# Kernel tuning notes

Measured on AMD Instinct MI355X. Metric: run time of the kernel, lower is better.

The kernel has to match this reference:

```python
import jax, jax.numpy as jnp
import numpy as np

B = 8192
H = 1024            # hidden_size
A = 512             # alphabet_size
S = 2               # sequence_length
D_IN = A * S        # 1024, gate input dim
D1, D2 = H // 2, H // 3   # decoder dims: 512, 341
TEMP = 1.0


def _linear_params(key, out_d, in_d):
    kw, kb = jax.random.split(key)
    lim = 1.0 / np.sqrt(in_d)
    W = jax.random.uniform(kw, (out_d, in_d), minval=-lim, maxval=lim, dtype=jnp.float32)
    b = jax.random.uniform(kb, (out_d,), minval=-lim, maxval=lim, dtype=jnp.float32)
    return W, b


def setup_inputs() -> dict:
    key = jax.random.key(0)
    ks = jax.random.split(key, 16)
    inp = {
        'x': jax.random.normal(ks[0], (B, D_IN), dtype=jnp.float32),
        'h': jax.random.normal(ks[1], (B, H), dtype=jnp.float32),
        'c': jax.random.normal(ks[2], (B, H), dtype=jnp.float32),
    }
    names = [('W_fi', 'b_fi', H, D_IN), ('W_fh', 'b_fh', H, H),
             ('W_ii', 'b_ii', H, D_IN), ('W_ih', 'b_ih', H, H),
             ('W_si', 'b_si', H, D_IN), ('W_sh', 'b_sh', H, H),
             ('W_oi', 'b_oi', H, D_IN), ('W_oh', 'b_oh', H, H),
             ('W_d1', 'b_d1', D1, H), ('W_d2', 'b_d2', D2, D1),
             ('W_d3', 'b_d3', A, D2)]
    for k, (wn, bn, od, idm) in zip(ks[3:3 + len(names)], names):
        W, b = _linear_params(k, od, idm)
        inp[wn] = W
        inp[bn] = b
    return inp


def reference(x, h, c,
              W_fi, b_fi, W_fh, b_fh,
              W_ii, b_ii, W_ih, b_ih,
              W_si, b_si, W_sh, b_sh,
              W_oi, b_oi, W_oh, b_oh,
              W_d1, b_d1, W_d2, b_d2, W_d3, b_d3):
    def lin(v, W, b):
        return v @ W.T + b

    f = jax.nn.sigmoid(lin(x, W_fi, b_fi) + lin(h, W_fh, b_fh))
    i = jax.nn.sigmoid(lin(x, W_ii, b_ii) + lin(h, W_ih, b_ih))
    s = jnp.tanh(lin(x, W_si, b_si) + lin(h, W_sh, b_sh))
    o = jax.nn.sigmoid(lin(x, W_oi, b_oi) + lin(h, W_oh, b_oh))
    c_new = c * f + i * s
    h_new = o * jnp.tanh(c_new)
    d = jnp.tanh(lin(h_new, W_d1, b_d1))
    d = jnp.tanh(lin(d, W_d2, b_d2))
    d = jax.nn.softmax(lin(d, W_d3, b_d3) / TEMP, axis=-1)
    return h_new, d
```

## Files before the change

### kernel.cpp

```cpp
#include <hip/hip_runtime.h>
#include <cstdint>
#include <cstddef>


typedef _Float16 half_t;
typedef _Float16 half8 __attribute__((ext_vector_type(8)));
typedef _Float16 half4v __attribute__((ext_vector_type(4)));
typedef float float4v __attribute__((ext_vector_type(4)));

#define GLD_LDS16(gptr, lptr)                                                  \
  __builtin_amdgcn_global_load_lds(                                            \
      (const __attribute__((address_space(1))) void*)(gptr),                   \
      (__attribute__((address_space(3))) void*)(lptr), 16, 0, 0)

__device__ __forceinline__ float fsig(float x) {
  return 1.0f / (1.0f + __expf(-x));
}
__device__ __forceinline__ float ftanh_(float x) {
  const float e = __expf(2.0f * x);
  return 1.0f - 2.0f / (e + 1.0f);
}

template <int TM, int ACT_TANH, int HALF_OUT>
__global__ __launch_bounds__(256) void gemm_f16(const half_t* __restrict__ A,
                                                const half_t* __restrict__ Bw,
                                                const float* __restrict__ bias,
                                                void* __restrict__ Cp,
                                                int N, int K) {
  constexpr int ASZ = TM * 64;
  constexpr int NPASS = (ASZ + 8192) / 4096;
  constexpr int JW = (TM == 128) ? 4 : 2;
  __shared__ alignas(16) half_t As[TM * 32];
  __shared__ alignas(16) half_t Bs[128 * 32];
  const int tid = threadIdx.x;
  const int lane = tid & 63;
  const int wave = tid >> 6;
  const size_t tile_m = (size_t)blockIdx.y * TM;
  const size_t tile_n = (size_t)blockIdx.x * 128;
  const int wm = (TM == 128) ? (wave >> 1) * 64 : 0;
  const int wn = (TM == 128) ? (wave & 1) * 64 : wave * 32;

  const half_t* gp[NPASS];
  half_t* lbase[NPASS];
  int lofs[NPASS];
#pragma unroll
  for (int s = 0; s < NPASS; ++s) {
    const int p = s * 4096 + tid * 16;
    if (p < ASZ) {
      const int r = p >> 6, cc = (p & 63) >> 1;
      gp[s] = A + (tile_m + r) * (size_t)K + cc;
      lbase[s] = As; lofs[s] = p;
    } else {
      const int q = p - ASZ;
      const int r = q >> 6, cc = (q & 63) >> 1;
      gp[s] = Bw + (tile_n + r) * (size_t)K + cc;
      lbase[s] = Bs; lofs[s] = q;
    }
  }

  float4v acc[4][JW] = {};
  for (int k0 = 0; k0 < K; k0 += 32) {
    __syncthreads();
#pragma unroll
    for (int s = 0; s < NPASS; ++s) GLD_LDS16(gp[s] + k0, (char*)lbase[s] + lofs[s]);
    __syncthreads();
    const int kh = (lane >> 4) * 8;
    half8 af[4], bf[JW];
#pragma unroll
    for (int i = 0; i < 4; ++i)
      af[i] = *(const half8*)(As + (wm + i * 16 + (lane & 15)) * 32 + kh);
#pragma unroll
    for (int j = 0; j < JW; ++j)
      bf[j] = *(const half8*)(Bs + (wn + j * 16 + (lane & 15)) * 32 + kh);
#pragma unroll
    for (int i = 0; i < 4; ++i)
#pragma unroll
      for (int j = 0; j < JW; ++j)
        acc[i][j] =
            __builtin_amdgcn_mfma_f32_16x16x32_f16(af[i], bf[j], acc[i][j], 0, 0, 0);
  }

  const size_t mb = tile_m + wm + ((lane >> 4) << 2);
  const size_t nb = tile_n + wn + (lane & 15);
#pragma unroll
  for (int j = 0; j < JW; ++j) {
    const size_t n = nb + j * 16;
    const float bv = bias[n];
#pragma unroll
    for (int i = 0; i < 4; ++i) {
#pragma unroll
      for (int r = 0; r < 4; ++r) {
        float v = acc[i][j][r] + bv;
        if (ACT_TANH) v = ftanh_(v);
        const size_t off = (mb + i * 16 + r) * (size_t)N + n;
        if (HALF_OUT)
          ((half_t*)Cp)[off] = (half_t)v;
        else
          ((float*)Cp)[off] = v;
      }
    }
  }
}

__global__ __launch_bounds__(256) void gemm_gates(const half_t* __restrict__ A,
                                                  const half_t* __restrict__ Bw,
                                                  const float* __restrict__ bias,
                                                  const float* __restrict__ cin,
                                                  float* __restrict__ hout,
                                                  half_t* __restrict__ h2) {
  constexpr int K = 2048;
  __shared__ alignas(16) half_t As[128 * 32];
  __shared__ alignas(16) half_t Bs[128 * 32];
  const int tid = threadIdx.x;
  const int lane = tid & 63;
  const int wave = tid >> 6;
  const size_t tile_m = (size_t)blockIdx.y * 128;
  const size_t tile_n = (size_t)blockIdx.x * 128;
  const int wm = (wave >> 1) * 64;
  const int wn = (wave & 1) * 64;

  const int p0 = tid * 16;
  const int p1 = 4096 + tid * 16;
  const int r0 = p0 >> 6, c0 = (p0 & 63) >> 1;
  const int r1 = p1 >> 6, c1 = (p1 & 63) >> 1;
  const half_t* Ag0 = A + (tile_m + r0) * (size_t)K + c0;
  const half_t* Ag1 = A + (tile_m + r1) * (size_t)K + c1;
  const half_t* Bg0 = Bw + (tile_n + r0) * (size_t)K + c0;
  const half_t* Bg1 = Bw + (tile_n + r1) * (size_t)K + c1;

  float4v acc[4][4] = {};
  for (int k0 = 0; k0 < K; k0 += 32) {
    __syncthreads();
    GLD_LDS16(Ag0 + k0, (char*)As + p0);
    GLD_LDS16(Ag1 + k0, (char*)As + p1);
    GLD_LDS16(Bg0 + k0, (char*)Bs + p0);
    GLD_LDS16(Bg1 + k0, (char*)Bs + p1);
    __syncthreads();
    const int kh = (lane >> 4) * 8;
    half8 af[4], bf[4];
#pragma unroll
    for (int i = 0; i < 4; ++i)
      af[i] = *(const half8*)(As + (wm + i * 16 + (lane & 15)) * 32 + kh);
#pragma unroll
    for (int j = 0; j < 4; ++j)
      bf[j] = *(const half8*)(Bs + (wn + j * 16 + (lane & 15)) * 32 + kh);
#pragma unroll
    for (int i = 0; i < 4; ++i)
#pragma unroll
      for (int j = 0; j < 4; ++j)
        acc[i][j] =
            __builtin_amdgcn_mfma_f32_16x16x32_f16(af[i], bf[j], acc[i][j], 0, 0, 0);
  }

  const int l = lane & 15;
  const int quad = lane >> 4;
  const int nwave = (int)tile_n + wn;
  const size_t u = (size_t)((nwave >> 6) << 4) + l;
  float bg[4];
#pragma unroll
  for (int g = 0; g < 4; ++g) bg[g] = bias[nwave + g * 16 + l];
#pragma unroll
  for (int i = 0; i < 4; ++i) {
#pragma unroll
    for (int r = 0; r < 4; ++r) {
      const size_t row = tile_m + wm + quad * 4 + i * 16 + r;
      const size_t off = row * 1024 + u;
      const float F = fsig(acc[i][0][r] + bg[0]);
      const float I = fsig(acc[i][1][r] + bg[1]);
      const float S = ftanh_(acc[i][2][r] + bg[2]);
      const float O = fsig(acc[i][3][r] + bg[3]);
      const float cn = cin[off] * F + I * S;
      const float hn = O * ftanh_(cn);
      hout[off] = hn;
      h2[off] = (half_t)hn;
    }
  }
}

__global__ void prep_pack(const float* __restrict__ x, const float* __restrict__ h,
                          const float* __restrict__ Wfi, const float* __restrict__ Wfh,
                          const float* __restrict__ Wii, const float* __restrict__ Wih,
                          const float* __restrict__ Wsi, const float* __restrict__ Wsh,
                          const float* __restrict__ Woi, const float* __restrict__ Woh,
                          half_t* __restrict__ xh, half_t* __restrict__ wall) {
  const int bid = blockIdx.x;
  const float* src;
  half_t* dst;
  size_t idx;
  if (bid < 16384) {
    idx = ((size_t)bid * 256 + threadIdx.x) * 4;
    const size_t b = idx >> 11;
    const int col = (int)(idx & 2047);
    src = (col < 1024) ? (x + b * 1024 + col) : (h + b * 1024 + (col - 1024));
    dst = xh + idx;
  } else {
    idx = ((size_t)(bid - 16384) * 256 + threadIdx.x) * 4;
    const int n = (int)(idx >> 11);
    const int col = (int)(idx & 2047);
    const int g = (n >> 4) & 3;
    const size_t u = (size_t)(((n >> 6) << 4) | (n & 15));
    const float* Wi = (g == 0) ? Wfi : (g == 1) ? Wii : (g == 2) ? Wsi : Woi;
    const float* Wh = (g == 0) ? Wfh : (g == 1) ? Wih : (g == 2) ? Wsh : Woh;
    src = (col < 1024) ? (Wi + u * 1024 + col) : (Wh + u * 1024 + (col - 1024));
    dst = wall + idx;
  }
  const float4v v = *(const float4v*)src;
  half4v o;
  o.x = (half_t)v.x; o.y = (half_t)v.y; o.z = (half_t)v.z; o.w = (half_t)v.w;
  *(half4v*)dst = o;
}

__global__ void prep_small(const float* __restrict__ Wd1, const float* __restrict__ Wd2,
                           const float* __restrict__ Wd3, const float* __restrict__ bd2,
                           const float* __restrict__ bfi, const float* __restrict__ bfh,
                           const float* __restrict__ bii, const float* __restrict__ bih,
                           const float* __restrict__ bsi, const float* __restrict__ bsh,
                           const float* __restrict__ boi, const float* __restrict__ boh,
                           half_t* __restrict__ WD1, half_t* __restrict__ WD2h,
                           half_t* __restrict__ WD3h, float* __restrict__ BALL,
                           float* __restrict__ BD2) {
  const int bid = blockIdx.x;
  const int tid = threadIdx.x;
  if (bid < 512) {
    const size_t i4 = ((size_t)bid * 256 + tid) * 4;
    const float4v v = *(const float4v*)(Wd1 + i4);
    half4v o;
    o.x = (half_t)v.x; o.y = (half_t)v.y; o.z = (half_t)v.z; o.w = (half_t)v.w;
    *(half4v*)(WD1 + i4) = o;
  } else if (bid < 704) {
    const size_t i4 = ((size_t)(bid - 512) * 256 + tid) * 4;
    const int r = (int)(i4 >> 9);
    const int cc = (int)(i4 & 511);
    half4v o;
    if (r < 341) {
      const float4v v = *(const float4v*)(Wd2 + (size_t)r * 512 + cc);
      o.x = (half_t)v.x; o.y = (half_t)v.y; o.z = (half_t)v.z; o.w = (half_t)v.w;
    } else {
      o.x = (half_t)0.f; o.y = (half_t)0.f; o.z = (half_t)0.f; o.w = (half_t)0.f;
    }
    *(half4v*)(WD2h + i4) = o;
  } else if (bid < 896) {
    const size_t i4 = ((size_t)(bid - 704) * 256 + tid) * 4;
    const int r = (int)(i4 / 384);
    const int cc = (int)(i4 - (size_t)r * 384);
    half4v o;
    o.x = (cc + 0 < 341) ? (half_t)Wd3[(size_t)r * 341 + cc + 0] : (half_t)0.f;
    o.y = (cc + 1 < 341) ? (half_t)Wd3[(size_t)r * 341 + cc + 1] : (half_t)0.f;
    o.z = (cc + 2 < 341) ? (half_t)Wd3[(size_t)r * 341 + cc + 2] : (half_t)0.f;
    o.w = (cc + 3 < 341) ? (half_t)Wd3[(size_t)r * 341 + cc + 3] : (half_t)0.f;
    *(half4v*)(WD3h + i4) = o;
  } else if (bid < 912) {
    const int n = (bid - 896) * 256 + tid;
    const int g = (n >> 4) & 3;
    const int u = ((n >> 6) << 4) | (n & 15);
    const float* bi = (g == 0) ? bfi : (g == 1) ? bii : (g == 2) ? bsi : boi;
    const float* bh = (g == 0) ? bfh : (g == 1) ? bih : (g == 2) ? bsh : boh;
    BALL[n] = bi[u] + bh[u];
  } else {
    const int i = (bid - 912) * 256 + tid;
    if (i < 384) BD2[i] = (i < 341) ? bd2[i] : 0.0f;
  }
}

__global__ __launch_bounds__(256) void softmax512(const float* __restrict__ logits,
                                                  float* __restrict__ out) {
  const int row = blockIdx.x * 4 + (threadIdx.x >> 6);
  const int lane = threadIdx.x & 63;
  const float4v* src = (const float4v*)(logits + (size_t)row * 512);
  const float4v v0 = src[lane * 2];
  const float4v v1 = src[lane * 2 + 1];
  float mx = fmaxf(fmaxf(fmaxf(v0.x, v0.y), fmaxf(v0.z, v0.w)),
                   fmaxf(fmaxf(v1.x, v1.y), fmaxf(v1.z, v1.w)));
#pragma unroll
  for (int off = 32; off > 0; off >>= 1) mx = fmaxf(mx, __shfl_xor(mx, off, 64));
  const float e0 = __expf(v0.x - mx), e1 = __expf(v0.y - mx);
  const float e2 = __expf(v0.z - mx), e3 = __expf(v0.w - mx);
  const float e4 = __expf(v1.x - mx), e5 = __expf(v1.y - mx);
  const float e6 = __expf(v1.z - mx), e7 = __expf(v1.w - mx);
  float sum = ((e0 + e1) + (e2 + e3)) + ((e4 + e5) + (e6 + e7));
#pragma unroll
  for (int off = 32; off > 0; off >>= 1) sum += __shfl_xor(sum, off, 64);
  const float inv = 1.0f / sum;
  float4v o0, o1;
  o0.x = e0 * inv; o0.y = e1 * inv; o0.z = e2 * inv; o0.w = e3 * inv;
  o1.x = e4 * inv; o1.y = e5 * inv; o1.z = e6 * inv; o1.w = e7 * inv;
  float4v* dst = (float4v*)(out + (size_t)row * 512);
  dst[lane * 2] = o0;
  dst[lane * 2 + 1] = o1;
}

extern "C" void kernel_launch(void* const* d_in, const int* in_sizes, int n_in,
                              void* d_out, int out_size, void* d_ws, size_t ws_size,
                              hipStream_t stream) {
  const float* x = (const float*)d_in[0];
  const float* h = (const float*)d_in[1];
  const float* c = (const float*)d_in[2];
  const float* Wfi = (const float*)d_in[3];  const float* bfi = (const float*)d_in[4];
  const float* Wfh = (const float*)d_in[5];  const float* bfh = (const float*)d_in[6];
  const float* Wii = (const float*)d_in[7];  const float* bii = (const float*)d_in[8];
  const float* Wih = (const float*)d_in[9];  const float* bih = (const float*)d_in[10];
  const float* Wsi = (const float*)d_in[11]; const float* bsi = (const float*)d_in[12];
  const float* Wsh = (const float*)d_in[13]; const float* bsh = (const float*)d_in[14];
  const float* Woi = (const float*)d_in[15]; const float* boi = (const float*)d_in[16];
  const float* Woh = (const float*)d_in[17]; const float* boh = (const float*)d_in[18];
  const float* Wd1 = (const float*)d_in[19]; const float* bd1 = (const float*)d_in[20];
  const float* Wd2 = (const float*)d_in[21]; const float* bd2 = (const float*)d_in[22];
  const float* Wd3 = (const float*)d_in[23]; const float* bd3 = (const float*)d_in[24];

  char* ws = (char*)d_ws;
  size_t o = 0;
  auto alloc = [&](size_t bytes) {
    size_t cur = o;
    o += (bytes + 255) & ~(size_t)255;
    return cur;
  };
  half_t* XH   = (half_t*)(ws + alloc((size_t)8192 * 2048 * 2));
  half_t* WALL = (half_t*)(ws + alloc((size_t)4096 * 2048 * 2));
  float*  BALL = (float*)(ws + alloc(4096 * 4));
  half_t* WD1  = (half_t*)(ws + alloc((size_t)512 * 1024 * 2));
  half_t* WD2  = (half_t*)(ws + alloc((size_t)384 * 512 * 2));
  float*  BD2  = (float*)(ws + alloc(384 * 4));
  half_t* WD3  = (half_t*)(ws + alloc((size_t)512 * 384 * 2));
  half_t* H2   = (half_t*)(ws + alloc((size_t)8192 * 1024 * 2));
  half_t* D1   = (half_t*)(ws + alloc((size_t)8192 * 512 * 2));
  half_t* D2   = (half_t*)(ws + alloc((size_t)8192 * 384 * 2));
  float*  LOG  = (float*)XH;

  float* h_out = (float*)d_out;
  float* d_outp = (float*)d_out + (size_t)8192 * 1024;

  prep_pack<<<24576, 256, 0, stream>>>(x, h, Wfi, Wfh, Wii, Wih, Wsi, Wsh, Woi, Woh,
                                       XH, WALL);
  prep_small<<<914, 256, 0, stream>>>(Wd1, Wd2, Wd3, bd2, bfi, bfh, bii, bih, bsi, bsh,
                                      boi, boh, WD1, WD2, WD3, BALL, BD2);

  gemm_gates<<<dim3(32, 64), 256, 0, stream>>>(XH, WALL, BALL, c, h_out, H2);

  gemm_f16<64, 1, 1><<<dim3(4, 128), 256, 0, stream>>>(H2, WD1, bd1, D1, 512, 1024);
  gemm_f16<64, 1, 1><<<dim3(3, 128), 256, 0, stream>>>(D1, WD2, BD2, D2, 384, 512);
  gemm_f16<64, 0, 0><<<dim3(4, 128), 256, 0, stream>>>(D2, WD3, bd3, LOG, 512, 384);
  softmax512<<<2048, 256, 0, stream>>>(LOG, d_outp);
}
```

Measured before the change: 446.2 us.

## Fuse decoder GEMMs and softmax into one kernel; swizzle gate GEMM LDS

Replaces the three decoder GEMM launches and the separate softmax with a single kernel that processes 16 rows per block, keeping intermediate activations in shared memory and doing a block-level softmax. It also applies an XOR swizzle to the LDS tile layout in the gate GEMM to reduce bank conflicts on fragment reads. This removes global round-trips for D1, D2 and the logits plus several launches. The cost is that every block re-streams all decoder weights with low reuse per block.

```diff
diff --git a/kernel.cpp b/kernel.cpp
--- a/kernel.cpp
+++ b/kernel.cpp
@@ -19,87 +19,6 @@
 __device__ __forceinline__ float ftanh_(float x) {
   const float e = __expf(2.0f * x);
   return 1.0f - 2.0f / (e + 1.0f);
-}
-
-template <int TM, int ACT_TANH, int HALF_OUT>
-__global__ __launch_bounds__(256) void gemm_f16(const half_t* __restrict__ A,
-                                                const half_t* __restrict__ Bw,
-                                                const float* __restrict__ bias,
-                                                void* __restrict__ Cp,
-                                                int N, int K) {
-  constexpr int ASZ = TM * 64;
-  constexpr int NPASS = (ASZ + 8192) / 4096;
-  constexpr int JW = (TM == 128) ? 4 : 2;
-  __shared__ alignas(16) half_t As[TM * 32];
-  __shared__ alignas(16) half_t Bs[128 * 32];
-  const int tid = threadIdx.x;
-  const int lane = tid & 63;
-  const int wave = tid >> 6;
-  const size_t tile_m = (size_t)blockIdx.y * TM;
-  const size_t tile_n = (size_t)blockIdx.x * 128;
-  const int wm = (TM == 128) ? (wave >> 1) * 64 : 0;
-  const int wn = (TM == 128) ? (wave & 1) * 64 : wave * 32;
-
-  const half_t* gp[NPASS];
-  half_t* lbase[NPASS];
-  int lofs[NPASS];
-#pragma unroll
-  for (int s = 0; s < NPASS; ++s) {
-    const int p = s * 4096 + tid * 16;
-    if (p < ASZ) {
-      const int r = p >> 6, cc = (p & 63) >> 1;
-      gp[s] = A + (tile_m + r) * (size_t)K + cc;
-      lbase[s] = As; lofs[s] = p;
-    } else {
-      const int q = p - ASZ;
-      const int r = q >> 6, cc = (q & 63) >> 1;
-      gp[s] = Bw + (tile_n + r) * (size_t)K + cc;
-      lbase[s] = Bs; lofs[s] = q;
-    }
-  }
-
-  float4v acc[4][JW] = {};
-  for (int k0 = 0; k0 < K; k0 += 32) {
-    __syncthreads();
-#pragma unroll
-    for (int s = 0; s < NPASS; ++s) GLD_LDS16(gp[s] + k0, (char*)lbase[s] + lofs[s]);
-    __syncthreads();
-    const int kh = (lane >> 4) * 8;
-    half8 af[4], bf[JW];
-#pragma unroll
-    for (int i = 0; i < 4; ++i)
-      af[i] = *(const half8*)(As + (wm + i * 16 + (lane & 15)) * 32 + kh);
-#pragma unroll
-    for (int j = 0; j < JW; ++j)
-      bf[j] = *(const half8*)(Bs + (wn + j * 16 + (lane & 15)) * 32 + kh);
-#pragma unroll
-    for (int i = 0; i < 4; ++i)
-#pragma unroll
-      for (int j = 0; j < JW; ++j)
-        acc[i][j] =
-            __builtin_amdgcn_mfma_f32_16x16x32_f16(af[i], bf[j], acc[i][j], 0, 0, 0);
-  }
-
-  const size_t mb = tile_m + wm + ((lane >> 4) << 2);
-  const size_t nb = tile_n + wn + (lane & 15);
-#pragma unroll
-  for (int j = 0; j < JW; ++j) {
-    const size_t n = nb + j * 16;
-    const float bv = bias[n];
-#pragma unroll
-    for (int i = 0; i < 4; ++i) {
-#pragma unroll
-      for (int r = 0; r < 4; ++r) {
-        float v = acc[i][j][r] + bv;
-        if (ACT_TANH) v = ftanh_(v);
-        const size_t off = (mb + i * 16 + r) * (size_t)N + n;
-        if (HALF_OUT)
-          ((half_t*)Cp)[off] = (half_t)v;
-        else
-          ((float*)Cp)[off] = v;
-      }
-    }
-  }
 }
 
 __global__ __launch_bounds__(256) void gemm_gates(const half_t* __restrict__ A,
@@ -114,19 +33,21 @@
   const int tid = threadIdx.x;
   const int lane = tid & 63;
   const int wave = tid >> 6;
+  const int m = lane & 15;
+  const int q = lane >> 4;
+  const int sx = (m >> 1) & 3;
   const size_t tile_m = (size_t)blockIdx.y * 128;
   const size_t tile_n = (size_t)blockIdx.x * 128;
   const int wm = (wave >> 1) * 64;
   const int wn = (wave & 1) * 64;
 
-  const int p0 = tid * 16;
-  const int p1 = 4096 + tid * 16;
-  const int r0 = p0 >> 6, c0 = (p0 & 63) >> 1;
-  const int r1 = p1 >> 6, c1 = (p1 & 63) >> 1;
-  const half_t* Ag0 = A + (tile_m + r0) * (size_t)K + c0;
-  const half_t* Ag1 = A + (tile_m + r1) * (size_t)K + c1;
-  const half_t* Bg0 = Bw + (tile_n + r0) * (size_t)K + c0;
-  const half_t* Bg1 = Bw + (tile_n + r1) * (size_t)K + c1;
+  const int cA0 = tid, rA0 = cA0 >> 2, kA0 = ((cA0 & 3) ^ ((rA0 >> 1) & 3));
+  const int cA1 = 256 + tid, rA1 = cA1 >> 2, kA1 = ((cA1 & 3) ^ ((rA1 >> 1) & 3));
+  const half_t* Ag0 = A + (tile_m + rA0) * (size_t)K + kA0 * 8;
+  const half_t* Ag1 = A + (tile_m + rA1) * (size_t)K + kA1 * 8;
+  const half_t* Bg0 = Bw + (tile_n + rA0) * (size_t)K + kA0 * 8;
+  const half_t* Bg1 = Bw + (tile_n + rA1) * (size_t)K + kA1 * 8;
+  const int p0 = cA0 * 16, p1 = cA1 * 16;
 
   float4v acc[4][4] = {};
   for (int k0 = 0; k0 < K; k0 += 32) {
@@ -136,14 +57,14 @@
     GLD_LDS16(Bg0 + k0, (char*)Bs + p0);
     GLD_LDS16(Bg1 + k0, (char*)Bs + p1);
     __syncthreads();
-    const int kh = (lane >> 4) * 8;
+    const int ks = (q ^ sx) * 8;
     half8 af[4], bf[4];
 #pragma unroll
     for (int i = 0; i < 4; ++i)
-      af[i] = *(const half8*)(As + (wm + i * 16 + (lane & 15)) * 32 + kh);
+      af[i] = *(const half8*)(As + (wm + i * 16 + m) * 32 + ks);
 #pragma unroll
     for (int j = 0; j < 4; ++j)
-      bf[j] = *(const half8*)(Bs + (wn + j * 16 + (lane & 15)) * 32 + kh);
+      bf[j] = *(const half8*)(Bs + (wn + j * 16 + m) * 32 + ks);
 #pragma unroll
     for (int i = 0; i < 4; ++i)
 #pragma unroll
@@ -152,18 +73,16 @@
             __builtin_amdgcn_mfma_f32_16x16x32_f16(af[i], bf[j], acc[i][j], 0, 0, 0);
   }
 
-  const int l = lane & 15;
-  const int quad = lane >> 4;
   const int nwave = (int)tile_n + wn;
-  const size_t u = (size_t)((nwave >> 6) << 4) + l;
+  const size_t u = (size_t)((nwave >> 6) << 4) + m;
   float bg[4];
 #pragma unroll
-  for (int g = 0; g < 4; ++g) bg[g] = bias[nwave + g * 16 + l];
+  for (int g = 0; g < 4; ++g) bg[g] = bias[nwave + g * 16 + m];
 #pragma unroll
   for (int i = 0; i < 4; ++i) {
 #pragma unroll
     for (int r = 0; r < 4; ++r) {
-      const size_t row = tile_m + wm + quad * 4 + i * 16 + r;
+      const size_t row = tile_m + wm + q * 4 + i * 16 + r;
       const size_t off = row * 1024 + u;
       const float F = fsig(acc[i][0][r] + bg[0]);
       const float I = fsig(acc[i][1][r] + bg[1]);
@@ -173,6 +92,186 @@
       const float hn = O * ftanh_(cn);
       hout[off] = hn;
       h2[off] = (half_t)hn;
+    }
+  }
+}
+
+__global__ __launch_bounds__(512) void decoder_fused(
+    const half_t* __restrict__ H2,
+    const half_t* __restrict__ W1,
+    const float* __restrict__ b1,
+    const half_t* __restrict__ W2,
+    const float* __restrict__ b2,
+    const half_t* __restrict__ W3,
+    const float* __restrict__ b3,
+    float* __restrict__ out) {
+  __shared__ alignas(16) half_t Bs[512 * 32];
+  __shared__ alignas(16) half_t As[16 * 40];
+  __shared__ alignas(16) half_t d1s[16 * 520];
+  __shared__ alignas(16) half_t d2s[16 * 392];
+  __shared__ float red[8 * 16];
+  __shared__ float rowred[16];
+
+  const int tid = threadIdx.x;
+  const int lane = tid & 63;
+  const int w = tid >> 6;
+  const int m = lane & 15;
+  const int q = lane >> 4;
+  const int sx = (m >> 1) & 3;
+  const size_t r0 = (size_t)blockIdx.x * 16;
+
+  {
+    float4v acc[4] = {};
+    for (int kk = 0; kk < 1024; kk += 32) {
+      __syncthreads();
+#pragma unroll
+      for (int p = 0; p < 4; ++p) {
+        const int cch = p * 512 + tid;
+        const int n = cch >> 2;
+        const int kq = (cch & 3) ^ ((n >> 1) & 3);
+        GLD_LDS16(W1 + (size_t)n * 1024 + kk + kq * 8, (char*)Bs + cch * 16);
+      }
+      if (tid < 64) {
+        const int row = tid >> 2;
+        const int kq = tid & 3;
+        const half8 v = *(const half8*)(H2 + (r0 + row) * 1024 + kk + kq * 8);
+        *(half8*)(As + row * 40 + kq * 8) = v;
+      }
+      __syncthreads();
+      const int ks = (q ^ sx) * 8;
+      const half8 af = *(const half8*)(As + m * 40 + q * 8);
+      half8 bf[4];
+#pragma unroll
+      for (int j = 0; j < 4; ++j)
+        bf[j] = *(const half8*)(Bs + (w * 64 + j * 16 + m) * 32 + ks);
+#pragma unroll
+      for (int j = 0; j < 4; ++j)
+        acc[j] = __builtin_amdgcn_mfma_f32_16x16x32_f16(af, bf[j], acc[j], 0, 0, 0);
+    }
+#pragma unroll
+    for (int j = 0; j < 4; ++j) {
+      const int col = w * 64 + j * 16 + m;
+      const float bv = b1[col];
+#pragma unroll
+      for (int r = 0; r < 4; ++r)
+        d1s[(q * 4 + r) * 520 + col] = (half_t)ftanh_(acc[j][r] + bv);
+    }
+  }
+
+  {
+    float4v acc[3] = {};
+    for (int kk = 0; kk < 512; kk += 32) {
+      __syncthreads();
+#pragma unroll
+      for (int p = 0; p < 3; ++p) {
+        const int cch = p * 512 + tid;
+        const int n = cch >> 2;
+        const int kq = (cch & 3) ^ ((n >> 1) & 3);
+        GLD_LDS16(W2 + (size_t)n * 512 + kk + kq * 8, (char*)Bs + cch * 16);
+      }
+      __syncthreads();
+      const int ks = (q ^ sx) * 8;
+      const half8 af = *(const half8*)(d1s + m * 520 + kk + q * 8);
+      half8 bf[3];
+#pragma unroll
+      for (int j = 0; j < 3; ++j)
+        bf[j] = *(const half8*)(Bs + (w * 48 + j * 16 + m) * 32 + ks);
+#pragma unroll
+      for (int j = 0; j < 3; ++j)
+        acc[j] = __builtin_amdgcn_mfma_f32_16x16x32_f16(af, bf[j], acc[j], 0, 0, 0);
+    }
+#pragma unroll
+    for (int j = 0; j < 3; ++j) {
+      const int col = w * 48 + j * 16 + m;
+      const float bv = b2[col];
+#pragma unroll
+      for (int r = 0; r < 4; ++r)
+        d2s[(q * 4 + r) * 392 + col] = (half_t)ftanh_(acc[j][r] + bv);
+    }
+  }
+
+  {
+    float4v acc[4] = {};
+    for (int kk = 0; kk < 384; kk += 32) {
+      __syncthreads();
+#pragma unroll
+      for (int p = 0; p < 4; ++p) {
+        const int cch = p * 512 + tid;
+        const int n = cch >> 2;
+        const int kq = (cch & 3) ^ ((n >> 1) & 3);
+        GLD_LDS16(W3 + (size_t)n * 384 + kk + kq * 8, (char*)Bs + cch * 16);
+      }
+      __syncthreads();
+      const int ks = (q ^ sx) * 8;
+      const half8 af = *(const half8*)(d2s + m * 392 + kk + q * 8);
+      half8 bf[4];
+#pragma unroll
+      for (int j = 0; j < 4; ++j)
+        bf[j] = *(const half8*)(Bs + (w * 64 + j * 16 + m) * 32 + ks);
+#pragma unroll
+      for (int j = 0; j < 4; ++j)
+        acc[j] = __builtin_amdgcn_mfma_f32_16x16x32_f16(af, bf[j], acc[j], 0, 0, 0);
+    }
+    float lg[4][4];
+#pragma unroll
+    for (int j = 0; j < 4; ++j) {
+      const float bv = b3[w * 64 + j * 16 + m];
+#pragma unroll
+      for (int r = 0; r < 4; ++r) lg[j][r] = acc[j][r] + bv;
+    }
+    float pmax[4];
+#pragma unroll
+    for (int r = 0; r < 4; ++r) {
+      float v = fmaxf(fmaxf(lg[0][r], lg[1][r]), fmaxf(lg[2][r], lg[3][r]));
+#pragma unroll
+      for (int d = 1; d < 16; d <<= 1) v = fmaxf(v, __shfl_xor(v, d, 64));
+      pmax[r] = v;
+    }
+    if (m == 0) {
+#pragma unroll
+      for (int r = 0; r < 4; ++r) red[w * 16 + q * 4 + r] = pmax[r];
+    }
+    __syncthreads();
+    if (tid < 16) {
+      float v = red[tid];
+#pragma unroll
+      for (int ww = 1; ww < 8; ++ww) v = fmaxf(v, red[ww * 16 + tid]);
+      rowred[tid] = v;
+    }
+    __syncthreads();
+    float ex[4][4], psum[4];
+#pragma unroll
+    for (int r = 0; r < 4; ++r) {
+      const float M = rowred[q * 4 + r];
+      float s = 0.f;
+#pragma unroll
+      for (int j = 0; j < 4; ++j) {
+        ex[j][r] = __expf(lg[j][r] - M);
+        s += ex[j][r];
+      }
+#pragma unroll
+      for (int d = 1; d < 16; d <<= 1) s += __shfl_xor(s, d, 64);
+      psum[r] = s;
+    }
+    if (m == 0) {
+#pragma unroll
+      for (int r = 0; r < 4; ++r) red[w * 16 + q * 4 + r] = psum[r];
+    }
+    __syncthreads();
+    if (tid < 16) {
+      float s = 0.f;
+#pragma unroll
+      for (int ww = 0; ww < 8; ++ww) s += red[ww * 16 + tid];
+      rowred[tid] = 1.0f / s;
+    }
+    __syncthreads();
+#pragma unroll
+    for (int r = 0; r < 4; ++r) {
+      const int row = q * 4 + r;
+      const float inv = rowred[row];
+#pragma unroll
+      for (int j = 0; j < 4; ++j)
+        out[(r0 + row) * 512 + w * 64 + j * 16 + m] = ex[j][r] * inv;
     }
   }
 }
@@ -262,33 +361,6 @@
   }
 }
 
-__global__ __launch_bounds__(256) void softmax512(const float* __restrict__ logits,
-                                                  float* __restrict__ out) {
-  const int row = blockIdx.x * 4 + (threadIdx.x >> 6);
-  const int lane = threadIdx.x & 63;
-  const float4v* src = (const float4v*)(logits + (size_t)row * 512);
-  const float4v v0 = src[lane * 2];
-  const float4v v1 = src[lane * 2 + 1];
-  float mx = fmaxf(fmaxf(fmaxf(v0.x, v0.y), fmaxf(v0.z, v0.w)),
-                   fmaxf(fmaxf(v1.x, v1.y), fmaxf(v1.z, v1.w)));
-#pragma unroll
-  for (int off = 32; off > 0; off >>= 1) mx = fmaxf(mx, __shfl_xor(mx, off, 64));
-  const float e0 = __expf(v0.x - mx), e1 = __expf(v0.y - mx);
-  const float e2 = __expf(v0.z - mx), e3 = __expf(v0.w - mx);
-  const float e4 = __expf(v1.x - mx), e5 = __expf(v1.y - mx);
-  const float e6 = __expf(v1.z - mx), e7 = __expf(v1.w - mx);
-  float sum = ((e0 + e1) + (e2 + e3)) + ((e4 + e5) + (e6 + e7));
-#pragma unroll
-  for (int off = 32; off > 0; off >>= 1) sum += __shfl_xor(sum, off, 64);
-  const float inv = 1.0f / sum;
-  float4v o0, o1;
-  o0.x = e0 * inv; o0.y = e1 * inv; o0.z = e2 * inv; o0.w = e3 * inv;
-  o1.x = e4 * inv; o1.y = e5 * inv; o1.z = e6 * inv; o1.w = e7 * inv;
-  float4v* dst = (float4v*)(out + (size_t)row * 512);
-  dst[lane * 2] = o0;
-  dst[lane * 2 + 1] = o1;
-}
-
 extern "C" void kernel_launch(void* const* d_in, const int* in_sizes, int n_in,
                               void* d_out, int out_size, void* d_ws, size_t ws_size,
                               hipStream_t stream) {
@@ -322,9 +394,6 @@
   float*  BD2  = (float*)(ws + alloc(384 * 4));
   half_t* WD3  = (half_t*)(ws + alloc((size_t)512 * 384 * 2));
   half_t* H2   = (half_t*)(ws + alloc((size_t)8192 * 1024 * 2));
-  half_t* D1   = (half_t*)(ws + alloc((size_t)8192 * 512 * 2));
-  half_t* D2   = (half_t*)(ws + alloc((size_t)8192 * 384 * 2));
-  float*  LOG  = (float*)XH;
 
   float* h_out = (float*)d_out;
   float* d_outp = (float*)d_out + (size_t)8192 * 1024;
@@ -336,8 +405,5 @@
 
   gemm_gates<<<dim3(32, 64), 256, 0, stream>>>(XH, WALL, BALL, c, h_out, H2);
 
-  gemm_f16<64, 1, 1><<<dim3(4, 128), 256, 0, stream>>>(H2, WD1, bd1, D1, 512, 1024);
-  gemm_f16<64, 1, 1><<<dim3(3, 128), 256, 0, stream>>>(D1, WD2, BD2, D2, 384, 512);
-  gemm_f16<64, 0, 0><<<dim3(4, 128), 256, 0, stream>>>(D2, WD3, bd3, LOG, 512, 384);
-  softmax512<<<2048, 256, 0, stream>>>(LOG, d_outp);
-}
+  decoder_fused<<<512, 512, 0, stream>>>(H2, WD1, bd1, WD2, BD2, WD3, bd3, d_outp);
+}
```

After: 449.4 us. No clear change (+0.7%).

## Store activations in MFMA-fragment layout and add weight-stationary decoder kernel

Applied to the files above, without the earlier changes.

The gates GEMM now writes h_new (fp16) straight into a fragment-packed layout. This lets each decoder layer load its A operand directly from global memory into registers without staging through LDS. A new dec_layer kernel keeps a 32-column weight slice in padded LDS and streams the packed activations, replacing the generic tiled gemm_f16. The gates kernel also gains an XOR swizzle on its LDS tiles to cut bank conflicts, and an XCD-aware block remap of its 1D grid. The trade-off is more, smaller blocks per decoder layer and a weight slice reloaded by every block.

```diff
diff --git a/kernel.cpp b/kernel.cpp
--- a/kernel.cpp
+++ b/kernel.cpp
@@ -19,87 +19,6 @@
 __device__ __forceinline__ float ftanh_(float x) {
   const float e = __expf(2.0f * x);
   return 1.0f - 2.0f / (e + 1.0f);
-}
-
-template <int TM, int ACT_TANH, int HALF_OUT>
-__global__ __launch_bounds__(256) void gemm_f16(const half_t* __restrict__ A,
-                                                const half_t* __restrict__ Bw,
-                                                const float* __restrict__ bias,
-                                                void* __restrict__ Cp,
-                                                int N, int K) {
-  constexpr int ASZ = TM * 64;
-  constexpr int NPASS = (ASZ + 8192) / 4096;
-  constexpr int JW = (TM == 128) ? 4 : 2;
-  __shared__ alignas(16) half_t As[TM * 32];
-  __shared__ alignas(16) half_t Bs[128 * 32];
-  const int tid = threadIdx.x;
-  const int lane = tid & 63;
-  const int wave = tid >> 6;
-  const size_t tile_m = (size_t)blockIdx.y * TM;
-  const size_t tile_n = (size_t)blockIdx.x * 128;
-  const int wm = (TM == 128) ? (wave >> 1) * 64 : 0;
-  const int wn = (TM == 128) ? (wave & 1) * 64 : wave * 32;
-
-  const half_t* gp[NPASS];
-  half_t* lbase[NPASS];
-  int lofs[NPASS];
-#pragma unroll
-  for (int s = 0; s < NPASS; ++s) {
-    const int p = s * 4096 + tid * 16;
-    if (p < ASZ) {
-      const int r = p >> 6, cc = (p & 63) >> 1;
-      gp[s] = A + (tile_m + r) * (size_t)K + cc;
-      lbase[s] = As; lofs[s] = p;
-    } else {
-      const int q = p - ASZ;
-      const int r = q >> 6, cc = (q & 63) >> 1;
-      gp[s] = Bw + (tile_n + r) * (size_t)K + cc;
-      lbase[s] = Bs; lofs[s] = q;
-    }
-  }
-
-  float4v acc[4][JW] = {};
-  for (int k0 = 0; k0 < K; k0 += 32) {
-    __syncthreads();
-#pragma unroll
-    for (int s = 0; s < NPASS; ++s) GLD_LDS16(gp[s] + k0, (char*)lbase[s] + lofs[s]);
-    __syncthreads();
-    const int kh = (lane >> 4) * 8;
-    half8 af[4], bf[JW];
-#pragma unroll
-    for (int i = 0; i < 4; ++i)
-      af[i] = *(const half8*)(As + (wm + i * 16 + (lane & 15)) * 32 + kh);
-#pragma unroll
-    for (int j = 0; j < JW; ++j)
-      bf[j] = *(const half8*)(Bs + (wn + j * 16 + (lane & 15)) * 32 + kh);
-#pragma unroll
-    for (int i = 0; i < 4; ++i)
-#pragma unroll
-      for (int j = 0; j < JW; ++j)
-        acc[i][j] =
-            __builtin_amdgcn_mfma_f32_16x16x32_f16(af[i], bf[j], acc[i][j], 0, 0, 0);
-  }
-
-  const size_t mb = tile_m + wm + ((lane >> 4) << 2);
-  const size_t nb = tile_n + wn + (lane & 15);
-#pragma unroll
-  for (int j = 0; j < JW; ++j) {
-    const size_t n = nb + j * 16;
-    const float bv = bias[n];
-#pragma unroll
-    for (int i = 0; i < 4; ++i) {
-#pragma unroll
-      for (int r = 0; r < 4; ++r) {
-        float v = acc[i][j][r] + bv;
-        if (ACT_TANH) v = ftanh_(v);
-        const size_t off = (mb + i * 16 + r) * (size_t)N + n;
-        if (HALF_OUT)
-          ((half_t*)Cp)[off] = (half_t)v;
-        else
-          ((float*)Cp)[off] = v;
-      }
-    }
-  }
 }
 
 __global__ __launch_bounds__(256) void gemm_gates(const half_t* __restrict__ A,
@@ -107,26 +26,32 @@
                                                   const float* __restrict__ bias,
                                                   const float* __restrict__ cin,
                                                   float* __restrict__ hout,
-                                                  half_t* __restrict__ h2) {
+                                                  half_t* __restrict__ h2f) {
   constexpr int K = 2048;
   __shared__ alignas(16) half_t As[128 * 32];
   __shared__ alignas(16) half_t Bs[128 * 32];
   const int tid = threadIdx.x;
   const int lane = tid & 63;
   const int wave = tid >> 6;
-  const size_t tile_m = (size_t)blockIdx.y * 128;
-  const size_t tile_n = (size_t)blockIdx.x * 128;
+  const int m = lane & 15;
+  const int q = lane >> 4;
+  const int sx = (m >> 1) & 3;
+
+  const int bid = blockIdx.x;
+  const int xcd = bid & 7;
+  const int l = bid >> 3;
+  const size_t tile_n = (size_t)((xcd << 2) | (l & 3)) * 128;
+  const size_t tile_m = (size_t)(l >> 2) * 128;
   const int wm = (wave >> 1) * 64;
   const int wn = (wave & 1) * 64;
 
-  const int p0 = tid * 16;
-  const int p1 = 4096 + tid * 16;
-  const int r0 = p0 >> 6, c0 = (p0 & 63) >> 1;
-  const int r1 = p1 >> 6, c1 = (p1 & 63) >> 1;
-  const half_t* Ag0 = A + (tile_m + r0) * (size_t)K + c0;
-  const half_t* Ag1 = A + (tile_m + r1) * (size_t)K + c1;
-  const half_t* Bg0 = Bw + (tile_n + r0) * (size_t)K + c0;
-  const half_t* Bg1 = Bw + (tile_n + r1) * (size_t)K + c1;
+  const int cA0 = tid, rA0 = cA0 >> 2, kA0 = ((cA0 & 3) ^ ((rA0 >> 1) & 3));
+  const int cA1 = 256 + tid, rA1 = cA1 >> 2, kA1 = ((cA1 & 3) ^ ((rA1 >> 1) & 3));
+  const half_t* Ag0 = A + (tile_m + rA0) * (size_t)K + kA0 * 8;
+  const half_t* Ag1 = A + (tile_m + rA1) * (size_t)K + kA1 * 8;
+  const half_t* Bg0 = Bw + (tile_n + rA0) * (size_t)K + kA0 * 8;
+  const half_t* Bg1 = Bw + (tile_n + rA1) * (size_t)K + kA1 * 8;
+  const int p0 = cA0 * 16, p1 = cA1 * 16;
 
   float4v acc[4][4] = {};
   for (int k0 = 0; k0 < K; k0 += 32) {
@@ -136,14 +61,14 @@
     GLD_LDS16(Bg0 + k0, (char*)Bs + p0);
     GLD_LDS16(Bg1 + k0, (char*)Bs + p1);
     __syncthreads();
-    const int kh = (lane >> 4) * 8;
+    const int ks = (q ^ sx) * 8;
     half8 af[4], bf[4];
 #pragma unroll
     for (int i = 0; i < 4; ++i)
-      af[i] = *(const half8*)(As + (wm + i * 16 + (lane & 15)) * 32 + kh);
+      af[i] = *(const half8*)(As + (wm + i * 16 + m) * 32 + ks);
 #pragma unroll
     for (int j = 0; j < 4; ++j)
-      bf[j] = *(const half8*)(Bs + (wn + j * 16 + (lane & 15)) * 32 + kh);
+      bf[j] = *(const half8*)(Bs + (wn + j * 16 + m) * 32 + ks);
 #pragma unroll
     for (int i = 0; i < 4; ++i)
 #pragma unroll
@@ -152,18 +77,18 @@
             __builtin_amdgcn_mfma_f32_16x16x32_f16(af[i], bf[j], acc[i][j], 0, 0, 0);
   }
 
-  const int l = lane & 15;
-  const int quad = lane >> 4;
   const int nwave = (int)tile_n + wn;
-  const size_t u = (size_t)((nwave >> 6) << 4) + l;
+  const int u = ((nwave >> 6) << 4) + m;
+  const int rtb = (int)((tile_m + wm) >> 4);
+  const int ubase = (u >> 5) * 512 + ((u >> 3) & 3) * 128 + (u & 7);
   float bg[4];
 #pragma unroll
-  for (int g = 0; g < 4; ++g) bg[g] = bias[nwave + g * 16 + l];
+  for (int g = 0; g < 4; ++g) bg[g] = bias[nwave + g * 16 + m];
 #pragma unroll
   for (int i = 0; i < 4; ++i) {
 #pragma unroll
     for (int r = 0; r < 4; ++r) {
-      const size_t row = tile_m + wm + quad * 4 + i * 16 + r;
+      const size_t row = tile_m + wm + q * 4 + i * 16 + r;
       const size_t off = row * 1024 + u;
       const float F = fsig(acc[i][0][r] + bg[0]);
       const float I = fsig(acc[i][1][r] + bg[1]);
@@ -172,9 +97,104 @@
       const float cn = cin[off] * F + I * S;
       const float hn = O * ftanh_(cn);
       hout[off] = hn;
-      h2[off] = (half_t)hn;
+      h2f[(size_t)(rtb + i) * 16384 + ubase + (q * 4 + r) * 8] = (half_t)hn;
     }
   }
+}
+
+template <int K, int OUTK, int MODE>
+__global__ __launch_bounds__(256) void dec_layer(const half_t* __restrict__ Af,
+                                                 const half_t* __restrict__ W,
+                                                 const float* __restrict__ bias,
+                                                 void* __restrict__ outp) {
+  constexpr int KP = K + 8;
+  constexpr int CH = K / 8;
+  constexpr int ITER = 32 * CH / 256;
+  __shared__ alignas(16) half_t Wl[32 * KP];
+  const int tid = threadIdx.x;
+  const int lane = tid & 63;
+  const int w = tid >> 6;
+  const int m = lane & 15;
+  const int q = lane >> 4;
+  const int g = blockIdx.x;
+
+#pragma unroll
+  for (int it = 0; it < ITER; ++it) {
+    const int ci = it * 256 + tid;
+    const int c = ci / CH;
+    const int kq = ci - c * CH;
+    const half8 v = *(const half8*)(W + ((size_t)(g * 32 + c)) * K + kq * 8);
+    *(half8*)(Wl + c * KP + kq * 8) = v;
+  }
+  __syncthreads();
+
+  const int rt0 = blockIdx.y * 8 + w * 2;
+  const half_t* a0 = Af + (size_t)rt0 * (16 * K) + lane * 8;
+  const half_t* a1 = a0 + 16 * K;
+  float4v acc[2][2] = {};
+#pragma unroll 2
+  for (int kk = 0; kk < K; kk += 32) {
+    const half8 af0 = *(const half8*)(a0 + kk * 16);
+    const half8 af1 = *(const half8*)(a1 + kk * 16);
+    half8 bf[2];
+#pragma unroll
+    for (int j = 0; j < 2; ++j)
+      bf[j] = *(const half8*)(Wl + (j * 16 + m) * KP + kk + q * 8);
+    acc[0][0] = __builtin_amdgcn_mfma_f32_16x16x32_f16(af0, bf[0], acc[0][0], 0, 0, 0);
+    acc[0][1] = __builtin_amdgcn_mfma_f32_16x16x32_f16(af0, bf[1], acc[0][1], 0, 0, 0);
+    acc[1][0] = __builtin_amdgcn_mfma_f32_16x16x32_f16(af1, bf[0], acc[1][0], 0, 0, 0);
+    acc[1][1] = __builtin_amdgcn_mfma_f32_16x16x32_f16(af1, bf[1], acc[1][1], 0, 0, 0);
+  }
+
+#pragma unroll
+  for (int t = 0; t < 2; ++t) {
+    const int rt = rt0 + t;
+#pragma unroll
+    for (int j = 0; j < 2; ++j) {
+      const int col = g * 32 + j * 16 + m;
+      const float bv = bias[col];
+      if (MODE == 0) {
+        half_t* of = (half_t*)outp;
+        const size_t base = (size_t)rt * (16 * OUTK) + g * 512 +
+                            (j * 2 + (m >> 3)) * 128 + (m & 7);
+#pragma unroll
+        for (int r = 0; r < 4; ++r)
+          of[base + (q * 4 + r) * 8] = (half_t)ftanh_(acc[t][j][r] + bv);
+      } else {
+        float* ol = (float*)outp;
+#pragma unroll
+        for (int r = 0; r < 4; ++r)
+          ol[((size_t)rt * 16 + q * 4 + r) * 512 + col] = acc[t][j][r] + bv;
+      }
+    }
+  }
+}
+
+__global__ __launch_bounds__(256) void softmax512(const float* __restrict__ logits,
+                                                  float* __restrict__ out) {
+  const int row = blockIdx.x * 4 + (threadIdx.x >> 6);
+  const int lane = threadIdx.x & 63;
+  const float4v* src = (const float4v*)(logits + (size_t)row * 512);
+  const float4v v0 = src[lane * 2];
+  const float4v v1 = src[lane * 2 + 1];
+  float mx = fmaxf(fmaxf(fmaxf(v0.x, v0.y), fmaxf(v0.z, v0.w)),
+                   fmaxf(fmaxf(v1.x, v1.y), fmaxf(v1.z, v1.w)));
+#pragma unroll
+  for (int off = 32; off > 0; off >>= 1) mx = fmaxf(mx, __shfl_xor(mx, off, 64));
+  const float e0 = __expf(v0.x - mx), e1 = __expf(v0.y - mx);
+  const float e2 = __expf(v0.z - mx), e3 = __expf(v0.w - mx);
+  const float e4 = __expf(v1.x - mx), e5 = __expf(v1.y - mx);
+  const float e6 = __expf(v1.z - mx), e7 = __expf(v1.w - mx);
+  float sum = ((e0 + e1) + (e2 + e3)) + ((e4 + e5) + (e6 + e7));
+#pragma unroll
+  for (int off = 32; off > 0; off >>= 1) sum += __shfl_xor(sum, off, 64);
+  const float inv = 1.0f / sum;
+  float4v o0, o1;
+  o0.x = e0 * inv; o0.y = e1 * inv; o0.z = e2 * inv; o0.w = e3 * inv;
+  o1.x = e4 * inv; o1.y = e5 * inv; o1.z = e6 * inv; o1.w = e7 * inv;
+  float4v* dst = (float4v*)(out + (size_t)row * 512);
+  dst[lane * 2] = o0;
+  dst[lane * 2 + 1] = o1;
 }
 
 __global__ void prep_pack(const float* __restrict__ x, const float* __restrict__ h,
@@ -262,33 +282,6 @@
   }
 }
 
-__global__ __launch_bounds__(256) void softmax512(const float* __restrict__ logits,
-                                                  float* __restrict__ out) {
-  const int row = blockIdx.x * 4 + (threadIdx.x >> 6);
-  const int lane = threadIdx.x & 63;
-  const float4v* src = (const float4v*)(logits + (size_t)row * 512);
-  const float4v v0 = src[lane * 2];
-  const float4v v1 = src[lane * 2 + 1];
-  float mx = fmaxf(fmaxf(fmaxf(v0.x, v0.y), fmaxf(v0.z, v0.w)),
-                   fmaxf(fmaxf(v1.x, v1.y), fmaxf(v1.z, v1.w)));
-#pragma unroll
-  for (int off = 32; off > 0; off >>= 1) mx = fmaxf(mx, __shfl_xor(mx, off, 64));
-  const float e0 = __expf(v0.x - mx), e1 = __expf(v0.y - mx);
-  const float e2 = __expf(v0.z - mx), e3 = __expf(v0.w - mx);
-  const float e4 = __expf(v1.x - mx), e5 = __expf(v1.y - mx);
-  const float e6 = __expf(v1.z - mx), e7 = __expf(v1.w - mx);
-  float sum = ((e0 + e1) + (e2 + e3)) + ((e4 + e5) + (e6 + e7));
-#pragma unroll
-  for (int off = 32; off > 0; off >>= 1) sum += __shfl_xor(sum, off, 64);
-  const float inv = 1.0f / sum;
-  float4v o0, o1;
-  o0.x = e0 * inv; o0.y = e1 * inv; o0.z = e2 * inv; o0.w = e3 * inv;
-  o1.x = e4 * inv; o1.y = e5 * inv; o1.z = e6 * inv; o1.w = e7 * inv;
-  float4v* dst = (float4v*)(out + (size_t)row * 512);
-  dst[lane * 2] = o0;
-  dst[lane * 2 + 1] = o1;
-}
-
 extern "C" void kernel_launch(void* const* d_in, const int* in_sizes, int n_in,
                               void* d_out, int out_size, void* d_ws, size_t ws_size,
                               hipStream_t stream) {
@@ -321,9 +314,9 @@
   half_t* WD2  = (half_t*)(ws + alloc((size_t)384 * 512 * 2));
   float*  BD2  = (float*)(ws + alloc(384 * 4));
   half_t* WD3  = (half_t*)(ws + alloc((size_t)512 * 384 * 2));
-  half_t* H2   = (half_t*)(ws + alloc((size_t)8192 * 1024 * 2));
-  half_t* D1   = (half_t*)(ws + alloc((size_t)8192 * 512 * 2));
-  half_t* D2   = (half_t*)(ws + alloc((size_t)8192 * 384 * 2));
+  half_t* H2F  = (half_t*)(ws + alloc((size_t)8192 * 1024 * 2));
+  half_t* D1F  = (half_t*)(ws + alloc((size_t)8192 * 512 * 2));
+  half_t* D2F  = (half_t*)(ws + alloc((size_t)8192 * 384 * 2));
   float*  LOG  = (float*)XH;
 
   float* h_out = (float*)d_out;
@@ -334,10 +327,10 @@
   prep_small<<<914, 256, 0, stream>>>(Wd1, Wd2, Wd3, bd2, bfi, bfh, bii, bih, bsi, bsh,
                                       boi, boh, WD1, WD2, WD3, BALL, BD2);
 
-  gemm_gates<<<dim3(32, 64), 256, 0, stream>>>(XH, WALL, BALL, c, h_out, H2);
-
-  gemm_f16<64, 1, 1><<<dim3(4, 128), 256, 0, stream>>>(H2, WD1, bd1, D1, 512, 1024);
-  gemm_f16<64, 1, 1><<<dim3(3, 128), 256, 0, stream>>>(D1, WD2, BD2, D2, 384, 512);
-  gemm_f16<64, 0, 0><<<dim3(4, 128), 256, 0, stream>>>(D2, WD3, bd3, LOG, 512, 384);
+  gemm_gates<<<2048, 256, 0, stream>>>(XH, WALL, BALL, c, h_out, H2F);
+
+  dec_layer<1024, 512, 0><<<dim3(16, 64), 256, 0, stream>>>(H2F, WD1, bd1, D1F);
+  dec_layer<512, 384, 0><<<dim3(12, 64), 256, 0, stream>>>(D1F, WD2, BD2, D2F);
+  dec_layer<384, 512, 1><<<dim3(16, 64), 256, 0, stream>>>(D2F, WD3, bd3, LOG);
   softmax512<<<2048, 256, 0, stream>>>(LOG, d_outp);
 }
```

Result: no change. 441.2 us (-1.1%).
